# Kernel optimization log

Hardware: AMD Instinct MI355X
Metric: run time of the kernel (lower is better)

Reference implementation:

```python
import jax, jax.numpy as jnp
import numpy as np

N, D, B, K, DOUT = 100000, 128, 500000, 3, 128


def setup_inputs() -> dict:
    key = jax.random.key(0)
    k1, k2, k3 = jax.random.split(key, 3)
    x = jax.random.normal(k1, (N, D), dtype=jnp.float32)
    indices = jax.random.randint(k2, (B, K), 0, N, dtype=jnp.int64)
    # xavier_normal_ for weight [D*(K+1), DOUT]
    fan_in, fan_out = D * (K + 1), DOUT
    std = float(np.sqrt(2.0 / (fan_in + fan_out)))
    weight = jax.random.normal(k3, (fan_in, fan_out), dtype=jnp.float32) * std
    return {"x": x, "indices": indices, "weight": weight}


def reference(x, indices, weight):
    # _1_to_k, cfg='default', normalize=False
    # gather K node rows per hyperedge and concat: [B, K*D]
    x_nonpool = x[indices].reshape(indices.shape[0], -1)
    w_nonpool = weight[:-D]          # [K*D, DOUT]
    w_pool = weight[-D:]             # [D, DOUT]
    x_pool = jnp.sum(x, axis=0, keepdims=True)  # [1, D] (sum since normalize=False)
    return x_nonpool @ w_nonpool + x_pool @ w_pool  # [B, DOUT]
```

## Files before the change

kernel.cpp:

```cpp
#include <hip/hip_runtime.h>
#include <stdint.h>

#define NROWS 100000
#define DIMD  128
#define KKIDX 3
#define NDOUT 128
#define KDIM  384
#define NBAT  500000

typedef float  f4v  __attribute__((ext_vector_type(4)));
typedef short  s8v  __attribute__((ext_vector_type(8)));
typedef unsigned int u4v __attribute__((ext_vector_type(4)));

__device__ __forceinline__ short f2bf(float f) {
    union { float f; uint32_t u; } c; c.f = f;
    uint32_t u = c.u;
    uint32_t r = (u + 0x7FFFu + ((u >> 16) & 1u)) >> 16;
    return (short)r;
}

__global__ void k_wt(const float* __restrict__ w, unsigned short* __restrict__ wT) {
    int g = blockIdx.x * 256 + threadIdx.x;
    if (g >= KDIM * NDOUT) return;
    int k = g >> 7;
    int n = g & 127;
    wT[n * KDIM + k] = (unsigned short)f2bf(w[g]);
}

template<bool WRITE_BF>
__global__ void k_colsum(const float* __restrict__ x, float* __restrict__ xpool,
                         unsigned short* __restrict__ xbf) {
    __shared__ float red[256];
    int col  = threadIdx.x & 127;
    int half = threadIdx.x >> 7;
    float acc = 0.f;
    int r0 = blockIdx.x * 250;
    for (int r = r0 + half; r < r0 + 250; r += 2) {
        float v = x[r * DIMD + col];
        acc += v;
        if (WRITE_BF) xbf[r * DIMD + col] = (unsigned short)f2bf(v);
    }
    red[threadIdx.x] = acc;
    __syncthreads();
    if (threadIdx.x < 128)
        atomicAdd(&xpool[col], red[threadIdx.x] + red[threadIdx.x + 128]);
}

__global__ void k_pool(const float* __restrict__ xpool, const float* __restrict__ w,
                       float* __restrict__ pool_out) {
    int j = threadIdx.x;
    float acc = 0.f;
    for (int d = 0; d < DIMD; ++d)
        acc += xpool[d] * w[(KDIM + d) * NDOUT + j];
    pool_out[j] = acc;
}

#define LSTR 200

template<bool XBF>
__global__ __launch_bounds__(512, 4)
void k_main(const float* __restrict__ x, const unsigned short* __restrict__ xbf,
            const int* __restrict__ idx, const unsigned short* __restrict__ wT,
            const float* __restrict__ pool, float* __restrict__ out) {
    __shared__ short wlds[128 * LSTR];
    const int tid  = threadIdx.x;
    const int wave = tid >> 6;
    const int lane = tid & 63;
    const int quad = lane >> 4;
    const int l16  = lane & 15;

    const int rowb = blockIdx.x * 256 + wave * 32;

    int goff[2][KKIDX];
    #pragma unroll
    for (int mt = 0; mt < 2; ++mt) {
        int r = rowb + mt * 16 + l16;
        if (r >= NBAT) r = NBAT - 1;
        #pragma unroll
        for (int s = 0; s < KKIDX; ++s)
            goff[mt][s] = idx[r * 3 + s] * DIMD;
    }

    f4v acc[2][8];
    #pragma unroll
    for (int mt = 0; mt < 2; ++mt)
        #pragma unroll
        for (int nt = 0; nt < 8; ++nt) {
            f4v z = {0.f, 0.f, 0.f, 0.f};
            acc[mt][nt] = z;
        }

    const int sn   = tid >> 2;
    const int sseg = tid & 3;

    s8v aC[2];
    #pragma unroll
    for (int mt = 0; mt < 2; ++mt) {
        if (XBF) {
            aC[mt] = *(const s8v*)(xbf + goff[mt][0] + quad * 8);
        } else {
            const float* ap = x + goff[mt][0] + quad * 8;
            f4v v0 = *(const f4v*)ap;
            f4v v1 = *(const f4v*)(ap + 4);
            s8v a;
            a[0] = f2bf(v0[0]); a[1] = f2bf(v0[1]);
            a[2] = f2bf(v0[2]); a[3] = f2bf(v0[3]);
            a[4] = f2bf(v1[0]); a[5] = f2bf(v1[1]);
            a[6] = f2bf(v1[2]); a[7] = f2bf(v1[3]);
            aC[mt] = a;
        }
    }

    #pragma unroll
    for (int p = 0; p < 2; ++p) {
        __syncthreads();
        #pragma unroll
        for (int j = 0; j < 6; ++j) {
            int k = sseg * 48 + j * 8;
            *(u4v*)(&wlds[sn * LSTR + k]) = *(const u4v*)(wT + sn * KDIM + p * 192 + k);
        }
        __syncthreads();

        #pragma unroll
        for (int ks = 0; ks < 6; ++ks) {
            const int kstep = p * 6 + ks;

            s8v aN[2];
            if (kstep < 11) {
                const int kn   = kstep + 1;
                const int srci = kn >> 2;
                const int colb = (kn & 3) * 32 + quad * 8;
                #pragma unroll
                for (int mt = 0; mt < 2; ++mt) {
                    if (XBF) {
                        aN[mt] = *(const s8v*)(xbf + goff[mt][srci] + colb);
                    } else {
                        const float* ap = x + goff[mt][srci] + colb;
                        f4v v0 = *(const f4v*)ap;
                        f4v v1 = *(const f4v*)(ap + 4);
                        s8v a;
                        a[0] = f2bf(v0[0]); a[1] = f2bf(v0[1]);
                        a[2] = f2bf(v0[2]); a[3] = f2bf(v0[3]);
                        a[4] = f2bf(v1[0]); a[5] = f2bf(v1[1]);
                        a[6] = f2bf(v1[2]); a[7] = f2bf(v1[3]);
                        aN[mt] = a;
                    }
                }
            }

            const int krow = ks * 32 + quad * 8;
            #pragma unroll
            for (int h = 0; h < 2; ++h) {
                s8v bF[4];
                #pragma unroll
                for (int q = 0; q < 4; ++q)
                    bF[q] = *(const s8v*)(&wlds[((h * 4 + q) * 16 + l16) * LSTR + krow]);
                #pragma unroll
                for (int mt = 0; mt < 2; ++mt)
                    #pragma unroll
                    for (int q = 0; q < 4; ++q)
                        acc[mt][h * 4 + q] = __builtin_amdgcn_mfma_f32_16x16x32_bf16(
                            bF[q], aC[mt], acc[mt][h * 4 + q], 0, 0, 0);
            }

            if (kstep < 11) { aC[0] = aN[0]; aC[1] = aN[1]; }
        }
    }

    #pragma unroll
    for (int nt = 0; nt < 8; ++nt) {
        f4v pv = *(const f4v*)(pool + nt * 16 + quad * 4);
        #pragma unroll
        for (int mt = 0; mt < 2; ++mt) {
            int r = rowb + mt * 16 + l16;
            if (r < NBAT) {
                f4v v = acc[mt][nt] + pv;
                __builtin_nontemporal_store(v,
                    (f4v*)(out + (size_t)r * NDOUT + nt * 16 + quad * 4));
            }
        }
    }
}

extern "C" void kernel_launch(void* const* d_in, const int* in_sizes, int n_in,
                              void* d_out, int out_size, void* d_ws, size_t ws_size,
                              hipStream_t stream) {
    const float* x   = (const float*)d_in[0];
    const int*   idx = (const int*)d_in[1];
    const float* w   = (const float*)d_in[2];
    float*       out = (float*)d_out;

    char* ws = (char*)d_ws;
    float* xpool           = (float*)ws;
    float* pool_out        = (float*)(ws + 512);
    unsigned short* wT     = (unsigned short*)(ws + 1024);
    unsigned short* xbf    = (unsigned short*)(ws + 99328);
    const size_t NEED_BIG  = 99328 + (size_t)NROWS * DIMD * 2;
    const bool big = ws_size >= NEED_BIG;

    hipMemsetAsync(xpool, 0, 512, stream);
    if (big) k_colsum<true ><<<400, 256, 0, stream>>>(x, xpool, xbf);
    else     k_colsum<false><<<400, 256, 0, stream>>>(x, xpool, xbf);
    k_wt  <<<192, 256, 0, stream>>>(w, wT);
    k_pool<<<1, 128, 0, stream>>>(xpool, w, pool_out);

    const int grid = (NBAT + 255) / 256;
    if (big) k_main<true ><<<grid, 512, 0, stream>>>(x, xbf, idx, wT, pool_out, out);
    else     k_main<false><<<grid, 512, 0, stream>>>(x, xbf, idx, wT, pool_out, out);
}
```

Before: 442.7 us.

## Split output columns across wave pairs, fuse prep kernels, drop atomics and memset

The main kernel now gives each pair of waves the same 32 rows, with each wave computing 64 of the 128 output columns. Each block therefore covers 128 rows instead of 256, and the accumulator count is halved so occupancy can rise (launch bounds go to 6). The column-sum and weight-transpose kernels are merged into one prep launch that writes per-block partial sums, replacing the memset and atomics, and k_pool reduces those partials. The cost is that every A fragment is now gathered by two waves instead of one, and each block's weight staging into LDS serves fewer rows.

Result: slower. 515.3 us (+16.4%).

```diff
diff --git a/kernel.cpp b/kernel.cpp
--- a/kernel.cpp
+++ b/kernel.cpp
@@ -19,17 +19,21 @@
     return (short)r;
 }
 
-__global__ void k_wt(const float* __restrict__ w, unsigned short* __restrict__ wT) {
-    int g = blockIdx.x * 256 + threadIdx.x;
-    if (g >= KDIM * NDOUT) return;
-    int k = g >> 7;
-    int n = g & 127;
-    wT[n * KDIM + k] = (unsigned short)f2bf(w[g]);
-}
-
 template<bool WRITE_BF>
-__global__ void k_colsum(const float* __restrict__ x, float* __restrict__ xpool,
-                         unsigned short* __restrict__ xbf) {
+__global__ void k_prep(const float* __restrict__ x, float* __restrict__ xpool_part,
+                       unsigned short* __restrict__ xbf,
+                       const float* __restrict__ w, unsigned short* __restrict__ wT) {
+    if (blockIdx.x >= 400) {
+        int b = blockIdx.x - 400;
+        #pragma unroll
+        for (int t = 0; t < 4; ++t) {
+            int g = b * 1024 + t * 256 + threadIdx.x;
+            int k = g >> 7;
+            int n = g & 127;
+            wT[n * KDIM + k] = (unsigned short)f2bf(w[g]);
+        }
+        return;
+    }
     __shared__ float red[256];
     int col  = threadIdx.x & 127;
     int half = threadIdx.x >> 7;
@@ -43,22 +47,27 @@
     red[threadIdx.x] = acc;
     __syncthreads();
     if (threadIdx.x < 128)
-        atomicAdd(&xpool[col], red[threadIdx.x] + red[threadIdx.x + 128]);
-}
-
-__global__ void k_pool(const float* __restrict__ xpool, const float* __restrict__ w,
+        xpool_part[blockIdx.x * 128 + threadIdx.x] = red[threadIdx.x] + red[threadIdx.x + 128];
+}
+
+__global__ void k_pool(const float* __restrict__ part, const float* __restrict__ w,
                        float* __restrict__ pool_out) {
+    __shared__ float xp[128];
     int j = threadIdx.x;
+    float s = 0.f;
+    for (int b = 0; b < 400; ++b) s += part[b * 128 + j];
+    xp[j] = s;
+    __syncthreads();
     float acc = 0.f;
     for (int d = 0; d < DIMD; ++d)
-        acc += xpool[d] * w[(KDIM + d) * NDOUT + j];
+        acc += xp[d] * w[(KDIM + d) * NDOUT + j];
     pool_out[j] = acc;
 }
 
 #define LSTR 200
 
 template<bool XBF>
-__global__ __launch_bounds__(512, 4)
+__global__ __launch_bounds__(512, 6)
 void k_main(const float* __restrict__ x, const unsigned short* __restrict__ xbf,
             const int* __restrict__ idx, const unsigned short* __restrict__ wT,
             const float* __restrict__ pool, float* __restrict__ out) {
@@ -69,7 +78,9 @@
     const int quad = lane >> 4;
     const int l16  = lane & 15;
 
-    const int rowb = blockIdx.x * 256 + wave * 32;
+    const int rowg = wave >> 1;
+    const int cbase = (wave & 1) * 64;
+    const int rowb = blockIdx.x * 128 + rowg * 32;
 
     int goff[2][KKIDX];
     #pragma unroll
@@ -81,11 +92,11 @@
             goff[mt][s] = idx[r * 3 + s] * DIMD;
     }
 
-    f4v acc[2][8];
+    f4v acc[2][4];
     #pragma unroll
     for (int mt = 0; mt < 2; ++mt)
         #pragma unroll
-        for (int nt = 0; nt < 8; ++nt) {
+        for (int nt = 0; nt < 4; ++nt) {
             f4v z = {0.f, 0.f, 0.f, 0.f};
             acc[mt][nt] = z;
         }
@@ -149,34 +160,31 @@
             }
 
             const int krow = ks * 32 + quad * 8;
+            s8v bF[4];
             #pragma unroll
-            for (int h = 0; h < 2; ++h) {
-                s8v bF[4];
+            for (int nt = 0; nt < 4; ++nt)
+                bF[nt] = *(const s8v*)(&wlds[(cbase + nt * 16 + l16) * LSTR + krow]);
+            #pragma unroll
+            for (int mt = 0; mt < 2; ++mt)
                 #pragma unroll
-                for (int q = 0; q < 4; ++q)
-                    bF[q] = *(const s8v*)(&wlds[((h * 4 + q) * 16 + l16) * LSTR + krow]);
-                #pragma unroll
-                for (int mt = 0; mt < 2; ++mt)
-                    #pragma unroll
-                    for (int q = 0; q < 4; ++q)
-                        acc[mt][h * 4 + q] = __builtin_amdgcn_mfma_f32_16x16x32_bf16(
-                            bF[q], aC[mt], acc[mt][h * 4 + q], 0, 0, 0);
-            }
+                for (int nt = 0; nt < 4; ++nt)
+                    acc[mt][nt] = __builtin_amdgcn_mfma_f32_16x16x32_bf16(
+                        bF[nt], aC[mt], acc[mt][nt], 0, 0, 0);
 
             if (kstep < 11) { aC[0] = aN[0]; aC[1] = aN[1]; }
         }
     }
 
     #pragma unroll
-    for (int nt = 0; nt < 8; ++nt) {
-        f4v pv = *(const f4v*)(pool + nt * 16 + quad * 4);
+    for (int nt = 0; nt < 4; ++nt) {
+        f4v pv = *(const f4v*)(pool + cbase + nt * 16 + quad * 4);
         #pragma unroll
         for (int mt = 0; mt < 2; ++mt) {
             int r = rowb + mt * 16 + l16;
             if (r < NBAT) {
                 f4v v = acc[mt][nt] + pv;
                 __builtin_nontemporal_store(v,
-                    (f4v*)(out + (size_t)r * NDOUT + nt * 16 + quad * 4));
+                    (f4v*)(out + (size_t)r * NDOUT + cbase + nt * 16 + quad * 4));
             }
         }
     }
@@ -191,20 +199,18 @@
     float*       out = (float*)d_out;
 
     char* ws = (char*)d_ws;
-    float* xpool           = (float*)ws;
-    float* pool_out        = (float*)(ws + 512);
-    unsigned short* wT     = (unsigned short*)(ws + 1024);
-    unsigned short* xbf    = (unsigned short*)(ws + 99328);
-    const size_t NEED_BIG  = 99328 + (size_t)NROWS * DIMD * 2;
+    float* pool_out        = (float*)ws;
+    float* xpool_part      = (float*)(ws + 512);
+    unsigned short* wT     = (unsigned short*)(ws + 205312);
+    unsigned short* xbf    = (unsigned short*)(ws + 303616);
+    const size_t NEED_BIG  = 303616 + (size_t)NROWS * DIMD * 2;
     const bool big = ws_size >= NEED_BIG;
 
-    hipMemsetAsync(xpool, 0, 512, stream);
-    if (big) k_colsum<true ><<<400, 256, 0, stream>>>(x, xpool, xbf);
-    else     k_colsum<false><<<400, 256, 0, stream>>>(x, xpool, xbf);
-    k_wt  <<<192, 256, 0, stream>>>(w, wT);
-    k_pool<<<1, 128, 0, stream>>>(xpool, w, pool_out);
-
-    const int grid = (NBAT + 255) / 256;
+    if (big) k_prep<true ><<<448, 256, 0, stream>>>(x, xpool_part, xbf, w, wT);
+    else     k_prep<false><<<448, 256, 0, stream>>>(x, xpool_part, xbf, w, wT);
+    k_pool<<<1, 128, 0, stream>>>(xpool_part, w, pool_out);
+
+    const int grid = (NBAT + 127) / 128;
     if (big) k_main<true ><<<grid, 512, 0, stream>>>(x, xbf, idx, wT, pool_out, out);
     else     k_main<false><<<grid, 512, 0, stream>>>(x, xbf, idx, wT, pool_out, out);
 }
```
